# Performance work log

Hardware: AMD Instinct MI355X
Metric: run time of the kernel (lower is better)

Reference implementation:

```python
import jax, jax.numpy as jnp
import numpy as np

B, S, D, H, DFF = 2, 2048, 1024, 16, 4096
DK = D // H
EPS = 1e-6


def layer_norm(x, alpha, bias):
    # TF reduce_std is biased std; eps added to std (not variance)
    mean = jnp.mean(x, axis=-1, keepdims=True)
    std = jnp.sqrt(jnp.mean((x - mean) ** 2, axis=-1, keepdims=True))
    return alpha * (x - mean) / (std + EPS) + bias


def setup_inputs() -> dict:
    key = jax.random.key(0)
    ks = jax.random.split(key, 10)
    s = 0.02
    return {
        "x": jax.random.normal(ks[0], (B, S, D), jnp.float32),
        "mask": jnp.ones((B, 1, 1, S), jnp.int32),
        "wq": jax.random.normal(ks[1], (D, D), jnp.float32) * s,
        "wk": jax.random.normal(ks[2], (D, D), jnp.float32) * s,
        "wv": jax.random.normal(ks[3], (D, D), jnp.float32) * s,
        "wo": jax.random.normal(ks[4], (D, D), jnp.float32) * s,
        "w1": jax.random.normal(ks[5], (D, DFF), jnp.float32) * s,
        "b1": jnp.zeros((DFF,), jnp.float32),
        "w2": jax.random.normal(ks[6], (DFF, D), jnp.float32) * s,
        "b2": jnp.zeros((D,), jnp.float32),
        "ln1_a": jnp.ones((D,), jnp.float32),
        "ln1_b": jnp.zeros((D,), jnp.float32),
        "ln2_a": jnp.ones((D,), jnp.float32),
        "ln2_b": jnp.zeros((D,), jnp.float32),
    }


def reference(x, mask, wq, wk, wv, wo, w1, b1, w2, b2, ln1_a, ln1_b, ln2_a, ln2_b):
    # --- residual 1: pre-norm self-attention ---
    xn = layer_norm(x, ln1_a, ln1_b)
    q = (xn @ wq).reshape(B, S, H, DK)
    k = (xn @ wk).reshape(B, S, H, DK)
    v = (xn @ wv).reshape(B, S, H, DK)
    scores = jnp.einsum('bqhd,bkhd->bhqk', q, k) / jnp.sqrt(jnp.float32(DK))
    scores = jnp.where(mask == 0, jnp.float32(-1e9), scores)
    attn = jax.nn.softmax(scores, axis=-1)  # dropout = identity at eval
    ctx = jnp.einsum('bhqk,bkhd->bqhd', attn, v).reshape(B, S, D)
    x = x + ctx @ wo
    # --- residual 2: pre-norm FFN ---
    xn = layer_norm(x, ln2_a, ln2_b)
    ff = jax.nn.relu(xn @ w1 + b1) @ w2 + b2
    return x + ff
```

## Files before the change

kernel.cpp:

```cpp
#include <hip/hip_runtime.h>

#define BATCH 2
#define SEQ   2048
#define DMODEL 1024
#define NHEAD 16
#define DHEAD 64
#define DFF_  4096
#define MROWS (BATCH*SEQ)
#define EPS 1e-6f

typedef unsigned short u16;
typedef unsigned int u32;
typedef __bf16 bf16x8 __attribute__((ext_vector_type(8)));
typedef float  f32x4  __attribute__((ext_vector_type(4)));
typedef u32    u32x2  __attribute__((ext_vector_type(2)));

__device__ __forceinline__ float bf2f(u16 h) {
    union { u32 u; float f; } v; v.u = ((u32)h) << 16; return v.f;
}
__device__ __forceinline__ u16 f2bf(float f) {
    union { float f; u32 u; } v; v.f = f;
    u32 u = v.u;
    u32 r = (u + 0x7fffu + ((u >> 16) & 1u)) >> 16;
    return (u16)r;
}

__device__ __forceinline__ void async16(const u16* g, u16* l) {
    __builtin_amdgcn_global_load_lds((const __attribute__((address_space(1))) void*)g,
                                     (__attribute__((address_space(3))) void*)l,
                                     16, 0, 0);
}

__global__ __launch_bounds__(256) void transpose_cvt(const float* __restrict__ in,
                                                     u16* __restrict__ out,
                                                     int R, int C) {
    __shared__ float tile[32][33];
    int c0 = blockIdx.x * 32, r0 = blockIdx.y * 32;
    int x = threadIdx.x, y = threadIdx.y;
    #pragma unroll
    for (int i = 0; i < 32; i += 8)
        tile[y + i][x] = in[(size_t)(r0 + y + i) * C + c0 + x];
    __syncthreads();
    #pragma unroll
    for (int i = 0; i < 32; i += 8)
        out[(size_t)(c0 + y + i) * R + r0 + x] = f2bf(tile[x][y + i]);
}

__global__ __launch_bounds__(256) void transpose_cvt4(const float* __restrict__ i0,
                                                      const float* __restrict__ i1,
                                                      const float* __restrict__ i2,
                                                      const float* __restrict__ i3,
                                                      u16* __restrict__ o0,
                                                      u16* __restrict__ o1,
                                                      u16* __restrict__ o2,
                                                      u16* __restrict__ o3) {
    __shared__ float tile[32][33];
    const float* in; u16* out;
    switch (blockIdx.z) {
        case 0: in = i0; out = o0; break;
        case 1: in = i1; out = o1; break;
        case 2: in = i2; out = o2; break;
        default: in = i3; out = o3; break;
    }
    int c0 = blockIdx.x * 32, r0 = blockIdx.y * 32;
    int x = threadIdx.x, y = threadIdx.y;
    #pragma unroll
    for (int i = 0; i < 32; i += 8)
        tile[y + i][x] = in[(size_t)(r0 + y + i) * DMODEL + c0 + x];
    __syncthreads();
    #pragma unroll
    for (int i = 0; i < 32; i += 8)
        out[(size_t)(c0 + y + i) * DMODEL + r0 + x] = f2bf(tile[x][y + i]);
}

__global__ __launch_bounds__(256) void transpose_v_perm(const u16* __restrict__ qkv,
                                                        u16* __restrict__ vtp) {
    __shared__ u16 tile[64][72];
    int kt = blockIdx.x * 64;
    int bh = blockIdx.y; int b = bh >> 4, h = bh & 15;
    const u16* in = qkv + ((size_t)(b * SEQ + kt)) * 3072 + 2 * DMODEL + h * DHEAD;
    u16* out = vtp + ((size_t)bh * DHEAD) * SEQ;
    int t = threadIdx.x;
    int r = t >> 3, c8 = (t & 7) * 8;
    #pragma unroll
    for (int pass = 0; pass < 2; pass++) {
        int row = r + pass * 32;
        uint4 v = *(const uint4*)(in + (size_t)row * 3072 + c8);
        *(uint4*)&tile[row][c8] = v;
    }
    __syncthreads();
    #pragma unroll
    for (int pass = 0; pass < 2; pass++) {
        int d = r + pass * 32;
        u16 o8[8];
        #pragma unroll
        for (int e = 0; e < 8; e++) {
            int c = c8 + e;
            o8[e] = tile[(c & 3) * 16 + (c >> 2)][d];
        }
        *(uint4*)(out + (size_t)d * SEQ + kt + c8) = *(const uint4*)o8;
    }
}

__global__ __launch_bounds__(256) void ln_kernel(const float* __restrict__ x,
                                                 const float* __restrict__ alpha,
                                                 const float* __restrict__ beta,
                                                 u16* __restrict__ out) {
    int row = blockIdx.x;
    int t = threadIdx.x;
    const float* xr = x + (size_t)row * DMODEL;
    float4 xv = ((const float4*)xr)[t];
    float f0 = xv.x, f1 = xv.y, f2 = xv.z, f3 = xv.w;
    float s1 = f0 + f1 + f2 + f3;
    float s2 = f0*f0 + f1*f1 + f2*f2 + f3*f3;
    #pragma unroll
    for (int off = 32; off >= 1; off >>= 1) {
        s1 += __shfl_xor(s1, off);
        s2 += __shfl_xor(s2, off);
    }
    __shared__ float r1[4], r2[4];
    int w = t >> 6, lane = t & 63;
    if (lane == 0) { r1[w] = s1; r2[w] = s2; }
    __syncthreads();
    s1 = r1[0] + r1[1] + r1[2] + r1[3];
    s2 = r2[0] + r2[1] + r2[2] + r2[3];
    float mean = s1 * (1.0f / DMODEL);
    float var  = s2 * (1.0f / DMODEL) - mean * mean;
    var = fmaxf(var, 0.0f);
    float inv = 1.0f / (sqrtf(var) + EPS);
    float4 av = ((const float4*)alpha)[t];
    float4 bv = ((const float4*)beta)[t];
    ushort4 ov;
    ov.x = f2bf(av.x * (f0 - mean) * inv + bv.x);
    ov.y = f2bf(av.y * (f1 - mean) * inv + bv.y);
    ov.z = f2bf(av.z * (f2 - mean) * inv + bv.z);
    ov.w = f2bf(av.w * (f3 - mean) * inv + bv.w);
    ((ushort4*)(out + (size_t)row * DMODEL))[t] = ov;
}

#define BK 64

template <int AI, int AJ, bool OUT_F32>
__global__ __launch_bounds__(256) void gemm_bt(const u16* __restrict__ A,
                                               const u16* __restrict__ BT,
                                               void* __restrict__ Cp,
                                               const float* __restrict__ bias,
                                               const float* __restrict__ residual,
                                               int M, int N, int K, int do_relu) {
    constexpr int BMt = AI * 32, BNt = AJ * 32;
    __shared__ u16 As[BMt * BK];
    __shared__ u16 Bs[BNt * BK];
    int t = threadIdx.x;
    int m0 = blockIdx.y * BMt, n0 = blockIdx.x * BNt;
    int lane = t & 63, w = t >> 6;
    int wr = w >> 1, wc = w & 1;
    int lhi = lane >> 4, llo = lane & 15;
    int sr = lane >> 3, sk = lane & 7;
    int skx = (sk ^ sr) * 8;

    f32x4 acc[AI][AJ] = {};

    const u16* Ab = A  + (size_t)m0 * K + skx;
    const u16* Bb = BT + (size_t)n0 * K + skx;

    for (int k0 = 0; k0 < K; k0 += BK) {
        __syncthreads();
        #pragma unroll
        for (int j = 0; j < AI; j++) {
            int blk = w * AI + j;
            async16(Ab + (size_t)(blk * 8 + sr) * K + k0, &As[blk * 512]);
        }
        #pragma unroll
        for (int j = 0; j < AJ; j++) {
            int blk = w * AJ + j;
            async16(Bb + (size_t)(blk * 8 + sr) * K + k0, &Bs[blk * 512]);
        }
        __syncthreads();
        #pragma unroll
        for (int kk = 0; kk < 2; kk++) {
            int slot = ((kk * 4 + lhi) ^ (llo & 7)) * 8;
            bf16x8 af[AI], bfr[AJ];
            #pragma unroll
            for (int i = 0; i < AI; i++)
                af[i]  = *(const bf16x8*)(&As[(wr * 16 * AI + i * 16 + llo) * 64 + slot]);
            #pragma unroll
            for (int j = 0; j < AJ; j++)
                bfr[j] = *(const bf16x8*)(&Bs[(wc * 16 * AJ + j * 16 + llo) * 64 + slot]);
            #pragma unroll
            for (int i = 0; i < AI; i++)
                #pragma unroll
                for (int j = 0; j < AJ; j++)
                    acc[i][j] = __builtin_amdgcn_mfma_f32_16x16x32_bf16(af[i], bfr[j], acc[i][j], 0, 0, 0);
        }
    }

    #pragma unroll
    for (int i = 0; i < AI; i++) {
        #pragma unroll
        for (int rr = 0; rr < 4; rr++) {
            int row = m0 + wr * 16 * AI + i * 16 + lhi * 4 + rr;
            #pragma unroll
            for (int j = 0; j < AJ; j++) {
                int col = n0 + wc * 16 * AJ + j * 16 + llo;
                float v = acc[i][j][rr];
                if (bias)      v += bias[col];
                if (residual)  v += residual[(size_t)row * N + col];
                if (do_relu)   v = fmaxf(v, 0.0f);
                size_t idx = (size_t)row * N + col;
                if (OUT_F32) ((float*)Cp)[idx] = v;
                else         ((u16*)Cp)[idx]   = f2bf(v);
            }
        }
    }
}

#define SCL 0.18033688f

__global__ __launch_bounds__(256) void flash_attn(const u16* __restrict__ qkv,
                                                  const u16* __restrict__ vtp,
                                                  const int* __restrict__ mask,
                                                  u16* __restrict__ ctx) {
    __shared__ u16 QPs[64 * 64];
    __shared__ u16 Ks[64 * 64];
    __shared__ u16 VTs[64 * 64];
    __shared__ float mbias[64];

    int t = threadIdx.x;
    int w = t >> 6, lane = t & 63, lhi = lane >> 4, llo = lane & 15;
    int sr = lane >> 3, sk = lane & 7;
    int skx = (sk ^ sr) * 8;
    int q0 = blockIdx.x * 64, h = blockIdx.y, b = blockIdx.z;

    const u16* Qg  = qkv + ((size_t)(b * SEQ + q0)) * 3072 + h * DHEAD;
    const u16* Kg  = qkv + ((size_t)(b * SEQ)) * 3072 + DMODEL + h * DHEAD;
    const u16* VTg = vtp + ((size_t)((b * NHEAD + h) * DHEAD)) * SEQ;

    #pragma unroll
    for (int j = 0; j < 2; j++) {
        int blk = w * 2 + j;
        async16(Qg + (size_t)(blk * 8 + sr) * 3072 + skx, &QPs[blk * 512]);
    }
    __syncthreads();
    bf16x8 qf[2];
    #pragma unroll
    for (int kk = 0; kk < 2; kk++)
        qf[kk] = *(const bf16x8*)&QPs[(w * 16 + llo) * 64 + ((kk * 4 + lhi) ^ (llo & 7)) * 8];

    u16* Ps = QPs + w * 1024;

    float l_part[4] = {};
    f32x4 o_acc[4] = {};

    for (int kt = 0; kt < SEQ; kt += 64) {
        __syncthreads();
        #pragma unroll
        for (int j = 0; j < 2; j++) {
            int blk = w * 2 + j;
            async16(Kg  + (size_t)(kt + blk * 8 + sr) * 3072 + skx, &Ks[blk * 512]);
            async16(VTg + (size_t)(blk * 8 + sr) * SEQ + kt + skx,  &VTs[blk * 512]);
        }
        if (t < 64) mbias[t] = (mask[b * SEQ + kt + t] == 0) ? -1.0e12f : 0.0f;
        __syncthreads();

        f32x4 s[4] = {};
        #pragma unroll
        for (int kk = 0; kk < 2; kk++) {
            #pragma unroll
            for (int j = 0; j < 4; j++) {
                bf16x8 kf = *(const bf16x8*)&Ks[(j * 16 + llo) * 64 +
                                                ((kk * 4 + lhi) ^ (llo & 7)) * 8];
                s[j] = __builtin_amdgcn_mfma_f32_16x16x32_bf16(qf[kk], kf, s[j], 0, 0, 0);
            }
        }
        float mb[4];
        #pragma unroll
        for (int j = 0; j < 4; j++) mb[j] = mbias[j * 16 + llo];

        #pragma unroll
        for (int rr = 0; rr < 4; rr++) {
            u32 pu[4];
            #pragma unroll
            for (int j = 0; j < 4; j++) {
                float p = __builtin_amdgcn_exp2f(__builtin_fmaf(s[j][rr], SCL, mb[j]));
                l_part[rr] += p;
                union { float f; u32 u; } c; c.f = p;
                pu[j] = c.u;
            }
            u32x2 pw;
            pw[0] = (pu[0] >> 16) | (pu[1] & 0xffff0000u);
            pw[1] = (pu[2] >> 16) | (pu[3] & 0xffff0000u);
            int prow = lhi * 4 + rr;
            *(u32x2*)&Ps[prow * 64 + ((llo >> 1) ^ (prow & 7)) * 8 + (llo & 1) * 4] = pw;
        }
        #pragma unroll
        for (int kk = 0; kk < 2; kk++) {
            bf16x8 pf = *(const bf16x8*)&Ps[llo * 64 + ((kk * 4 + lhi) ^ (llo & 7)) * 8];
            #pragma unroll
            for (int nb = 0; nb < 4; nb++) {
                bf16x8 vf = *(const bf16x8*)&VTs[(nb * 16 + llo) * 64 +
                                                 ((kk * 4 + lhi) ^ (llo & 7)) * 8];
                o_acc[nb] = __builtin_amdgcn_mfma_f32_16x16x32_bf16(pf, vf, o_acc[nb], 0, 0, 0);
            }
        }
    }

    #pragma unroll
    for (int rr = 0; rr < 4; rr++) {
        float l = l_part[rr];
        #pragma unroll
        for (int off = 1; off <= 8; off <<= 1) l += __shfl_xor(l, off);
        float inv = __builtin_amdgcn_rcpf(l);
        int row = q0 + w * 16 + lhi * 4 + rr;
        #pragma unroll
        for (int nb = 0; nb < 4; nb++) {
            int col = h * DHEAD + nb * 16 + llo;
            ctx[((size_t)(b * SEQ) + row) * DMODEL + col] = f2bf(o_acc[nb][rr] * inv);
        }
    }
}

extern "C" void kernel_launch(void* const* d_in, const int* in_sizes, int n_in,
                              void* d_out, int out_size, void* d_ws, size_t ws_size,
                              hipStream_t stream) {
    (void)in_sizes; (void)n_in; (void)out_size; (void)ws_size;
    const float* x    = (const float*)d_in[0];
    const int* mask   = (const int*)d_in[1];
    const float* wq   = (const float*)d_in[2];
    const float* wk   = (const float*)d_in[3];
    const float* wv   = (const float*)d_in[4];
    const float* wo   = (const float*)d_in[5];
    const float* w1   = (const float*)d_in[6];
    const float* b1   = (const float*)d_in[7];
    const float* w2   = (const float*)d_in[8];
    const float* b2   = (const float*)d_in[9];
    const float* ln1a = (const float*)d_in[10];
    const float* ln1b = (const float*)d_in[11];
    const float* ln2a = (const float*)d_in[12];
    const float* ln2b = (const float*)d_in[13];
    float* out = (float*)d_out;

    char* wsb = (char*)d_ws;
    const size_t MB = 1024 * 1024;
    u16*   wqkvT = (u16*)(wsb + 0);
    u16*   woT   = (u16*)(wsb + 6 * MB);
    u16*   w1T   = (u16*)(wsb + 8 * MB);
    u16*   w2T   = (u16*)(wsb + 16 * MB);
    u16*   xn    = (u16*)(wsb + 24 * MB);
    float* x2    = (float*)(wsb + 32 * MB);
    u16*   vtp   = (u16*)(wsb + 32 * MB);
    u16*   ctx   = (u16*)(wsb + 48 * MB);
    u16*   qkv   = (u16*)(wsb + 56 * MB);
    u16*   ff1   = (u16*)(wsb + 56 * MB);

    dim3 tb(32, 8);
    transpose_cvt4<<<dim3(DMODEL/32, DMODEL/32, 4), tb, 0, stream>>>(
        wq, wk, wv, wo,
        wqkvT, wqkvT + 1024*1024, wqkvT + 2*1024*1024, woT);
    transpose_cvt<<<dim3(DFF_/32,  DMODEL/32),  tb, 0, stream>>>(w1, w1T, DMODEL, DFF_);
    transpose_cvt<<<dim3(DMODEL/32, DFF_/32),   tb, 0, stream>>>(w2, w2T, DFF_, DMODEL);

    ln_kernel<<<MROWS, 256, 0, stream>>>(x, ln1a, ln1b, xn);
    gemm_bt<4,2,false><<<dim3(3072/64, MROWS/128), 256, 0, stream>>>(xn, wqkvT, qkv,
                                                                     nullptr, nullptr,
                                                                     MROWS, 3072, DMODEL, 0);
    transpose_v_perm<<<dim3(SEQ/64, BATCH*NHEAD), 256, 0, stream>>>(qkv, vtp);
    flash_attn<<<dim3(SEQ/64, NHEAD, BATCH), 256, 0, stream>>>(qkv, vtp, mask, ctx);
    gemm_bt<2,2,true><<<dim3(DMODEL/64, MROWS/64), 256, 0, stream>>>(ctx, woT, x2,
                                                                     nullptr, x,
                                                                     MROWS, DMODEL, DMODEL, 0);
    ln_kernel<<<MROWS, 256, 0, stream>>>(x2, ln2a, ln2b, xn);
    gemm_bt<4,2,false><<<dim3(DFF_/64, MROWS/128), 256, 0, stream>>>(xn, w1T, ff1,
                                                                    b1, nullptr,
                                                                    MROWS, DFF_, DMODEL, 1);
    gemm_bt<2,2,true><<<dim3(DMODEL/64, MROWS/64), 256, 0, stream>>>(ff1, w2T, out,
                                                                    b2, x2,
                                                                    MROWS, DMODEL, DFF_, 0);
}
```

Measured before the change: 387.9 us.

## Double-buffer K/V tiles in flash attention and keep mask bias in registers

The flash attention kernel now keeps two LDS buffers for the K and V^T tiles. It prefetches the next tile asynchronously while computing on the current one, which drops the loop to one barrier per iteration instead of two. The mask bias moves from a shared array to per-lane registers, with the next tile's mask loaded ahead of time. The aim is to hide global load latency behind MFMA work. The cost is roughly double the LDS footprint for K/V, which may lower occupancy.

```diff
diff --git a/kernel.cpp b/kernel.cpp
--- a/kernel.cpp
+++ b/kernel.cpp
@@ -221,9 +221,8 @@
                                                   const int* __restrict__ mask,
                                                   u16* __restrict__ ctx) {
     __shared__ u16 QPs[64 * 64];
-    __shared__ u16 Ks[64 * 64];
-    __shared__ u16 VTs[64 * 64];
-    __shared__ float mbias[64];
+    __shared__ u16 Ks[2][64 * 64];
+    __shared__ u16 VTs[2][64 * 64];
 
     int t = threadIdx.x;
     int w = t >> 6, lane = t & 63, lhi = lane >> 4, llo = lane & 15;
@@ -234,12 +233,20 @@
     const u16* Qg  = qkv + ((size_t)(b * SEQ + q0)) * 3072 + h * DHEAD;
     const u16* Kg  = qkv + ((size_t)(b * SEQ)) * 3072 + DMODEL + h * DHEAD;
     const u16* VTg = vtp + ((size_t)((b * NHEAD + h) * DHEAD)) * SEQ;
+    const int* mrow = mask + b * SEQ;
 
     #pragma unroll
     for (int j = 0; j < 2; j++) {
         int blk = w * 2 + j;
-        async16(Qg + (size_t)(blk * 8 + sr) * 3072 + skx, &QPs[blk * 512]);
-    }
+        async16(Qg  + (size_t)(blk * 8 + sr) * 3072 + skx, &QPs[blk * 512]);
+        async16(Kg  + (size_t)(blk * 8 + sr) * 3072 + skx, &Ks[0][blk * 512]);
+        async16(VTg + (size_t)(blk * 8 + sr) * SEQ + skx,  &VTs[0][blk * 512]);
+    }
+    float mbC[4];
+    #pragma unroll
+    for (int j = 0; j < 4; j++)
+        mbC[j] = (mrow[j * 16 + llo] == 0) ? -1.0e12f : 0.0f;
+
     __syncthreads();
     bf16x8 qf[2];
     #pragma unroll
@@ -250,38 +257,41 @@
 
     float l_part[4] = {};
     f32x4 o_acc[4] = {};
+    int cur = 0;
 
     for (int kt = 0; kt < SEQ; kt += 64) {
-        __syncthreads();
-        #pragma unroll
-        for (int j = 0; j < 2; j++) {
-            int blk = w * 2 + j;
-            async16(Kg  + (size_t)(kt + blk * 8 + sr) * 3072 + skx, &Ks[blk * 512]);
-            async16(VTg + (size_t)(blk * 8 + sr) * SEQ + kt + skx,  &VTs[blk * 512]);
-        }
-        if (t < 64) mbias[t] = (mask[b * SEQ + kt + t] == 0) ? -1.0e12f : 0.0f;
-        __syncthreads();
+        if (kt + 64 < SEQ) {
+            #pragma unroll
+            for (int j = 0; j < 2; j++) {
+                int blk = w * 2 + j;
+                async16(Kg  + (size_t)(kt + 64 + blk * 8 + sr) * 3072 + skx,
+                        &Ks[cur ^ 1][blk * 512]);
+                async16(VTg + (size_t)(blk * 8 + sr) * SEQ + (kt + 64) + skx,
+                        &VTs[cur ^ 1][blk * 512]);
+            }
+        }
+        int ktn = (kt + 64 < SEQ) ? (kt + 64) : 0;
+        int mvN[4];
+        #pragma unroll
+        for (int j = 0; j < 4; j++) mvN[j] = mrow[ktn + j * 16 + llo];
 
         f32x4 s[4] = {};
         #pragma unroll
         for (int kk = 0; kk < 2; kk++) {
             #pragma unroll
             for (int j = 0; j < 4; j++) {
-                bf16x8 kf = *(const bf16x8*)&Ks[(j * 16 + llo) * 64 +
-                                                ((kk * 4 + lhi) ^ (llo & 7)) * 8];
+                bf16x8 kf = *(const bf16x8*)&Ks[cur][(j * 16 + llo) * 64 +
+                                                    ((kk * 4 + lhi) ^ (llo & 7)) * 8];
                 s[j] = __builtin_amdgcn_mfma_f32_16x16x32_bf16(qf[kk], kf, s[j], 0, 0, 0);
             }
         }
-        float mb[4];
-        #pragma unroll
-        for (int j = 0; j < 4; j++) mb[j] = mbias[j * 16 + llo];
 
         #pragma unroll
         for (int rr = 0; rr < 4; rr++) {
             u32 pu[4];
             #pragma unroll
             for (int j = 0; j < 4; j++) {
-                float p = __builtin_amdgcn_exp2f(__builtin_fmaf(s[j][rr], SCL, mb[j]));
+                float p = __builtin_amdgcn_exp2f(__builtin_fmaf(s[j][rr], SCL, mbC[j]));
                 l_part[rr] += p;
                 union { float f; u32 u; } c; c.f = p;
                 pu[j] = c.u;
@@ -297,11 +307,18 @@
             bf16x8 pf = *(const bf16x8*)&Ps[llo * 64 + ((kk * 4 + lhi) ^ (llo & 7)) * 8];
             #pragma unroll
             for (int nb = 0; nb < 4; nb++) {
-                bf16x8 vf = *(const bf16x8*)&VTs[(nb * 16 + llo) * 64 +
-                                                 ((kk * 4 + lhi) ^ (llo & 7)) * 8];
+                bf16x8 vf = *(const bf16x8*)&VTs[cur][(nb * 16 + llo) * 64 +
+                                                      ((kk * 4 + lhi) ^ (llo & 7)) * 8];
                 o_acc[nb] = __builtin_amdgcn_mfma_f32_16x16x32_bf16(pf, vf, o_acc[nb], 0, 0, 0);
             }
         }
+
+        __syncthreads();
+        cur ^= 1;
+
+        #pragma unroll
+        for (int j = 0; j < 4; j++)
+            mbC[j] = (mvN[j] == 0) ? -1.0e12f : 0.0f;
     }
 
     #pragma unroll
```

New measurement: 379.0 us. 2.3% less time.

## Use 2 waves per attention block with 32 query rows each, reusing K fragments

Applied to the files above, without the earlier changes.

The flash attention kernel now runs 128 threads per block, and each wave handles 32 query rows (two 16-row groups) instead of 16. K and V fragments loaded from shared memory are reused across both row groups, which halves LDS reads per MFMA. The mask is read straight from global memory instead of being staged in shared memory, and s_setprio is raised around the MFMA sections. In exchange it uses more registers per wave and has fewer waves per block to hide latency.

```diff
diff --git a/kernel.cpp b/kernel.cpp
--- a/kernel.cpp
+++ b/kernel.cpp
@@ -216,14 +216,13 @@
 
 #define SCL 0.18033688f
 
-__global__ __launch_bounds__(256) void flash_attn(const u16* __restrict__ qkv,
+__global__ __launch_bounds__(128) void flash_attn(const u16* __restrict__ qkv,
                                                   const u16* __restrict__ vtp,
                                                   const int* __restrict__ mask,
                                                   u16* __restrict__ ctx) {
     __shared__ u16 QPs[64 * 64];
     __shared__ u16 Ks[64 * 64];
     __shared__ u16 VTs[64 * 64];
-    __shared__ float mbias[64];
 
     int t = threadIdx.x;
     int w = t >> 6, lane = t & 63, lhi = lane >> 4, llo = lane & 15;
@@ -234,89 +233,114 @@
     const u16* Qg  = qkv + ((size_t)(b * SEQ + q0)) * 3072 + h * DHEAD;
     const u16* Kg  = qkv + ((size_t)(b * SEQ)) * 3072 + DMODEL + h * DHEAD;
     const u16* VTg = vtp + ((size_t)((b * NHEAD + h) * DHEAD)) * SEQ;
-
-    #pragma unroll
-    for (int j = 0; j < 2; j++) {
-        int blk = w * 2 + j;
+    const int* mrow = mask + b * SEQ;
+
+    #pragma unroll
+    for (int j = 0; j < 4; j++) {
+        int blk = w * 4 + j;
         async16(Qg + (size_t)(blk * 8 + sr) * 3072 + skx, &QPs[blk * 512]);
     }
     __syncthreads();
-    bf16x8 qf[2];
-    #pragma unroll
-    for (int kk = 0; kk < 2; kk++)
-        qf[kk] = *(const bf16x8*)&QPs[(w * 16 + llo) * 64 + ((kk * 4 + lhi) ^ (llo & 7)) * 8];
-
-    u16* Ps = QPs + w * 1024;
-
-    float l_part[4] = {};
-    f32x4 o_acc[4] = {};
+    bf16x8 qf[2][2];
+    #pragma unroll
+    for (int g = 0; g < 2; g++)
+        #pragma unroll
+        for (int kk = 0; kk < 2; kk++)
+            qf[g][kk] = *(const bf16x8*)&QPs[(w * 32 + g * 16 + llo) * 64 +
+                                             ((kk * 4 + lhi) ^ (llo & 7)) * 8];
+
+    u16* Ps = QPs + w * 2048;
+
+    float l_part[2][4] = {};
+    f32x4 o_acc[2][4] = {};
 
     for (int kt = 0; kt < SEQ; kt += 64) {
         __syncthreads();
         #pragma unroll
-        for (int j = 0; j < 2; j++) {
-            int blk = w * 2 + j;
+        for (int j = 0; j < 4; j++) {
+            int blk = w * 4 + j;
             async16(Kg  + (size_t)(kt + blk * 8 + sr) * 3072 + skx, &Ks[blk * 512]);
             async16(VTg + (size_t)(blk * 8 + sr) * SEQ + kt + skx,  &VTs[blk * 512]);
         }
-        if (t < 64) mbias[t] = (mask[b * SEQ + kt + t] == 0) ? -1.0e12f : 0.0f;
         __syncthreads();
 
-        f32x4 s[4] = {};
+        float mb[4];
+        #pragma unroll
+        for (int j = 0; j < 4; j++)
+            mb[j] = (mrow[kt + j * 16 + llo] == 0) ? -1.0e12f : 0.0f;
+
+        bf16x8 kf[2][4];
+        #pragma unroll
+        for (int kk = 0; kk < 2; kk++)
+            #pragma unroll
+            for (int j = 0; j < 4; j++)
+                kf[kk][j] = *(const bf16x8*)&Ks[(j * 16 + llo) * 64 +
+                                                ((kk * 4 + lhi) ^ (llo & 7)) * 8];
+
+        f32x4 s[2][4] = {};
+        __builtin_amdgcn_s_setprio(1);
+        #pragma unroll
+        for (int kk = 0; kk < 2; kk++)
+            #pragma unroll
+            for (int j = 0; j < 4; j++) {
+                s[0][j] = __builtin_amdgcn_mfma_f32_16x16x32_bf16(qf[0][kk], kf[kk][j], s[0][j], 0, 0, 0);
+                s[1][j] = __builtin_amdgcn_mfma_f32_16x16x32_bf16(qf[1][kk], kf[kk][j], s[1][j], 0, 0, 0);
+            }
+        __builtin_amdgcn_s_setprio(0);
+
+        #pragma unroll
+        for (int g = 0; g < 2; g++)
+            #pragma unroll
+            for (int rr = 0; rr < 4; rr++) {
+                u32 pu[4];
+                #pragma unroll
+                for (int j = 0; j < 4; j++) {
+                    float p = __builtin_amdgcn_exp2f(__builtin_fmaf(s[g][j][rr], SCL, mb[j]));
+                    l_part[g][rr] += p;
+                    union { float f; u32 u; } c; c.f = p;
+                    pu[j] = c.u;
+                }
+                u32x2 pw;
+                pw[0] = (pu[0] >> 16) | (pu[1] & 0xffff0000u);
+                pw[1] = (pu[2] >> 16) | (pu[3] & 0xffff0000u);
+                int prow = g * 16 + lhi * 4 + rr;
+                *(u32x2*)&Ps[prow * 64 + ((llo >> 1) ^ (prow & 7)) * 8 + (llo & 1) * 4] = pw;
+            }
+
+        __builtin_amdgcn_s_setprio(1);
         #pragma unroll
         for (int kk = 0; kk < 2; kk++) {
-            #pragma unroll
-            for (int j = 0; j < 4; j++) {
-                bf16x8 kf = *(const bf16x8*)&Ks[(j * 16 + llo) * 64 +
-                                                ((kk * 4 + lhi) ^ (llo & 7)) * 8];
-                s[j] = __builtin_amdgcn_mfma_f32_16x16x32_bf16(qf[kk], kf, s[j], 0, 0, 0);
-            }
-        }
-        float mb[4];
-        #pragma unroll
-        for (int j = 0; j < 4; j++) mb[j] = mbias[j * 16 + llo];
-
-        #pragma unroll
-        for (int rr = 0; rr < 4; rr++) {
-            u32 pu[4];
-            #pragma unroll
-            for (int j = 0; j < 4; j++) {
-                float p = __builtin_amdgcn_exp2f(__builtin_fmaf(s[j][rr], SCL, mb[j]));
-                l_part[rr] += p;
-                union { float f; u32 u; } c; c.f = p;
-                pu[j] = c.u;
-            }
-            u32x2 pw;
-            pw[0] = (pu[0] >> 16) | (pu[1] & 0xffff0000u);
-            pw[1] = (pu[2] >> 16) | (pu[3] & 0xffff0000u);
-            int prow = lhi * 4 + rr;
-            *(u32x2*)&Ps[prow * 64 + ((llo >> 1) ^ (prow & 7)) * 8 + (llo & 1) * 4] = pw;
-        }
-        #pragma unroll
-        for (int kk = 0; kk < 2; kk++) {
-            bf16x8 pf = *(const bf16x8*)&Ps[llo * 64 + ((kk * 4 + lhi) ^ (llo & 7)) * 8];
+            bf16x8 pf[2];
+            #pragma unroll
+            for (int g = 0; g < 2; g++)
+                pf[g] = *(const bf16x8*)&Ps[(g * 16 + llo) * 64 +
+                                            ((kk * 4 + lhi) ^ (llo & 7)) * 8];
             #pragma unroll
             for (int nb = 0; nb < 4; nb++) {
                 bf16x8 vf = *(const bf16x8*)&VTs[(nb * 16 + llo) * 64 +
                                                  ((kk * 4 + lhi) ^ (llo & 7)) * 8];
-                o_acc[nb] = __builtin_amdgcn_mfma_f32_16x16x32_bf16(pf, vf, o_acc[nb], 0, 0, 0);
+                o_acc[0][nb] = __builtin_amdgcn_mfma_f32_16x16x32_bf16(pf[0], vf, o_acc[0][nb], 0, 0, 0);
+                o_acc[1][nb] = __builtin_amdgcn_mfma_f32_16x16x32_bf16(pf[1], vf, o_acc[1][nb], 0, 0, 0);
             }
         }
-    }
-
-    #pragma unroll
-    for (int rr = 0; rr < 4; rr++) {
-        float l = l_part[rr];
-        #pragma unroll
-        for (int off = 1; off <= 8; off <<= 1) l += __shfl_xor(l, off);
-        float inv = __builtin_amdgcn_rcpf(l);
-        int row = q0 + w * 16 + lhi * 4 + rr;
-        #pragma unroll
-        for (int nb = 0; nb < 4; nb++) {
-            int col = h * DHEAD + nb * 16 + llo;
-            ctx[((size_t)(b * SEQ) + row) * DMODEL + col] = f2bf(o_acc[nb][rr] * inv);
-        }
-    }
+        __builtin_amdgcn_s_setprio(0);
+    }
+
+    #pragma unroll
+    for (int g = 0; g < 2; g++)
+        #pragma unroll
+        for (int rr = 0; rr < 4; rr++) {
+            float l = l_part[g][rr];
+            #pragma unroll
+            for (int off = 1; off <= 8; off <<= 1) l += __shfl_xor(l, off);
+            float inv = __builtin_amdgcn_rcpf(l);
+            int row = q0 + w * 32 + g * 16 + lhi * 4 + rr;
+            #pragma unroll
+            for (int nb = 0; nb < 4; nb++) {
+                int col = h * DHEAD + nb * 16 + llo;
+                ctx[((size_t)(b * SEQ) + row) * DMODEL + col] = f2bf(o_acc[g][nb][rr] * inv);
+            }
+        }
 }
 
 extern "C" void kernel_launch(void* const* d_in, const int* in_sizes, int n_in,
@@ -364,7 +388,7 @@
                                                                      nullptr, nullptr,
                                                                      MROWS, 3072, DMODEL, 0);
     transpose_v_perm<<<dim3(SEQ/64, BATCH*NHEAD), 256, 0, stream>>>(qkv, vtp);
-    flash_attn<<<dim3(SEQ/64, NHEAD, BATCH), 256, 0, stream>>>(qkv, vtp, mask, ctx);
+    flash_attn<<<dim3(SEQ/64, NHEAD, BATCH), 128, 0, stream>>>(qkv, vtp, mask, ctx);
     gemm_bt<2,2,true><<<dim3(DMODEL/64, MROWS/64), 256, 0, stream>>>(ctx, woT, x2,
                                                                      nullptr, x,
                                                                      MROWS, DMODEL, DMODEL, 0);
```

Result: no change. 381.4 us (-1.7%).
